# Performance work log

Hardware: AMD Instinct MI355X
Metric: run time of the kernel (lower is better)

The kernel has to match this reference:

```python
import jax, jax.numpy as jnp
import numpy as np

D_MODEL = 1024
N_HEADS = 16
NEG_INF = -1e9


def setup_inputs() -> dict:
    key = jax.random.key(0)
    ks = jax.random.split(key, 12)
    B, S, D = 2, 2048, D_MODEL
    Q = jax.random.normal(ks[0], (B, S, D), jnp.float32)
    K = jax.random.normal(ks[1], (B, S, D), jnp.float32)
    V = jax.random.normal(ks[2], (B, S, D), jnp.float32)
    # causal mask (1 = attend, 0 = masked), per mask==0 -> -1e9 in the source
    mask = jnp.tril(jnp.ones((S, S), bool))[None, :, :].repeat(B, axis=0)
    sc = 1.0 / np.sqrt(D)
    Wq = jax.random.normal(ks[3], (D, D), jnp.float32) * sc
    bq = jnp.zeros((D,), jnp.float32)
    Wk = jax.random.normal(ks[4], (D, D), jnp.float32) * sc
    bk = jnp.zeros((D,), jnp.float32)
    Wv = jax.random.normal(ks[5], (D, D), jnp.float32) * sc
    bv = jnp.zeros((D,), jnp.float32)
    Wo = jax.random.normal(ks[6], (D, D), jnp.float32) * sc
    bo = jnp.zeros((D,), jnp.float32)
    return {"Q": Q, "K": K, "V": V, "mask": mask,
            "Wq": Wq, "bq": bq, "Wk": Wk, "bk": bk,
            "Wv": Wv, "bv": bv, "Wo": Wo, "bo": bo}


def reference(Q, K, V, mask, Wq, bq, Wk, bk, Wv, bv, Wo, bo):
    B, S, D = Q.shape
    H = N_HEADS
    dk = D // H
    scale = jnp.asarray(dk, Q.dtype) ** -0.5
    # projections (torch nn.Linear: x @ W^T + b), split heads -> [B,H,S,dk]
    q = (Q @ Wq.T + bq).reshape(B, S, H, dk).transpose(0, 2, 1, 3)
    k = (K @ Wk.T + bk).reshape(B, S, H, dk).transpose(0, 2, 1, 3)
    v = (V @ Wv.T + bv).reshape(B, S, H, dk).transpose(0, 2, 1, 3)
    scores = jnp.einsum('bhqd,bhkd->bhqk', q, k) * scale  # [B,H,S,S]
    scores = jnp.where(mask[:, None, :, :], scores, NEG_INF)
    attn = jax.nn.softmax(scores, axis=-1)
    # dropout is identity in eval mode
    out = jnp.einsum('bhqk,bhkd->bhqd', attn, v)
    out = out.transpose(0, 2, 1, 3).reshape(B, S, D)
    return out @ Wo.T + bo, attn
```

## Files before the change

### kernel.cpp

```cpp
#include <hip/hip_runtime.h>
#include <cstddef>
#include <cstdint>

typedef unsigned short u16;
typedef unsigned int   u32;
typedef __attribute__((ext_vector_type(8))) short          bf16x8;
typedef __attribute__((ext_vector_type(4))) float          f32x4;
typedef __attribute__((ext_vector_type(4))) unsigned short u16x4;

#define S_LEN 2048
#define DM    1024
#define NROWS 4096
#define QSCALE 0.18033688011112042f
#define SOFTC  28.853900817779268f

__device__ __forceinline__ u16 f2bf(float x) {
  u32 u = __float_as_uint(x);
  return (u16)((u + 0x7fffu + ((u >> 16) & 1u)) >> 16);
}
__device__ __forceinline__ float bf2f(u16 h) { return __uint_as_float(((u32)h) << 16); }
__device__ __forceinline__ u32 cvtpk(float lo, float hi) {
  u32 r; asm("v_cvt_pk_bf16_f32 %0, %1, %2" : "=v"(r) : "v"(lo), "v"(hi)); return r;
}
__device__ __forceinline__ void gld16(const void* g, void* l) {
  __builtin_amdgcn_global_load_lds((const __attribute__((address_space(1))) void*)g,
                                   (__attribute__((address_space(3))) void*)l, 16, 0, 0);
}
__device__ __forceinline__ int swz4(int r) { return (r & 3) ^ ((r >> 2) & 3); }
#define MFMA16(a,b,c) __builtin_amdgcn_mfma_f32_16x16x32_bf16(a,b,c,0,0,0)

struct SplitArgs { const float* s[7]; u16* h[7]; u16* l[7]; int n4[7]; };

__global__ __launch_bounds__(256) void splitk7(SplitArgs a) {
  const int y = blockIdx.y;
  const float* s = a.s[y];
  u16* h = a.h[y]; u16* l = a.l[y];
  const int n4 = a.n4[y];
  const int step = gridDim.x * 256;
  for (int i = blockIdx.x * 256 + threadIdx.x; i < n4; i += step) {
    float4 v = ((const float4*)s)[i];
    u16x4 hh, ll; u16 x;
    x = f2bf(v.x); hh[0] = x; ll[0] = f2bf(v.x - bf2f(x));
    x = f2bf(v.y); hh[1] = x; ll[1] = f2bf(v.y - bf2f(x));
    x = f2bf(v.z); hh[2] = x; ll[2] = f2bf(v.z - bf2f(x));
    x = f2bf(v.w); hh[3] = x; ll[3] = f2bf(v.w - bf2f(x));
    *(u16x4*)&h[(size_t)i * 4] = hh;
    *(u16x4*)&l[(size_t)i * 4] = ll;
  }
}

template<int EPI>
__global__ __launch_bounds__(256) void gemm_split(
    const u16* __restrict__ Ah, const u16* __restrict__ Al,
    const u16* __restrict__ Bh, const u16* __restrict__ Bl,
    const float* __restrict__ bias,
    u16* __restrict__ Oh, u16* __restrict__ Ol, float* __restrict__ Of,
    float scale)
{
  __shared__ __align__(16) u16 lds[2][16384];
  const int t = threadIdx.x;
  const int id = blockIdx.x;
  const int bn = (id & 7) * 128;
  const int bm = (id >> 3) * 128;
  const int lane = t & 63, w = t >> 6;
  const int u = lane >> 4, c15 = lane & 15;
  const int wr = (w >> 1) * 64, wc = (w & 1) * 64;

  f32x4 acc[4][4];
#pragma unroll
  for (int i = 0; i < 4; ++i)
#pragma unroll
    for (int j = 0; j < 4; ++j) acc[i][j] = (f32x4){0.f, 0.f, 0.f, 0.f};

  auto stage = [&](int buf, int kb) {
    u16* L = lds[buf];
#pragma unroll
    for (int pp = 0; pp < 2; ++pp) {
      const int q = t + pp * 256;
      const int row = q >> 2;
      const int ch = (q & 3) ^ swz4(row);
      const int co = kb + 8 * ch;
      gld16(Ah + (size_t)(bm + row) * DM + co, L + q * 8);
      gld16(Al + (size_t)(bm + row) * DM + co, L + 4096 + q * 8);
      gld16(Bh + (size_t)(bn + row) * DM + co, L + 8192 + q * 8);
      gld16(Bl + (size_t)(bn + row) * DM + co, L + 12288 + q * 8);
    }
  };

  stage(0, 0);
  __syncthreads();
  int buf = 0;
  for (int kb = 0; kb < DM; kb += 32) {
    if (kb + 32 < DM) stage(buf ^ 1, kb + 32);
    const u16* L = lds[buf];
    bf16x8 ah[4], al[4];
#pragma unroll
    for (int i = 0; i < 4; ++i) {
      const int r = wr + 16 * i + c15;
      const int off = r * 32 + 8 * (u ^ swz4(r));
      ah[i] = *(const bf16x8*)&L[off];
      al[i] = *(const bf16x8*)&L[4096 + off];
    }
#pragma unroll
    for (int j = 0; j < 4; ++j) {
      const int n = wc + 16 * j + c15;
      const int off = n * 32 + 8 * (u ^ swz4(n));
      bf16x8 bh8 = *(const bf16x8*)&L[8192 + off];
      bf16x8 bl8 = *(const bf16x8*)&L[12288 + off];
#pragma unroll
      for (int i = 0; i < 4; ++i) {
        acc[i][j] = MFMA16(ah[i], bh8, acc[i][j]);
        acc[i][j] = MFMA16(ah[i], bl8, acc[i][j]);
        acc[i][j] = MFMA16(al[i], bh8, acc[i][j]);
      }
    }
    __syncthreads();
    buf ^= 1;
  }

#pragma unroll
  for (int j = 0; j < 4; ++j) {
    const int n = bn + wc + 16 * j + c15;
    const float bv = bias[n];
#pragma unroll
    for (int i = 0; i < 4; ++i) {
      float v[4];
#pragma unroll
      for (int r = 0; r < 4; ++r) v[r] = (acc[i][j][r] + bv) * scale;
      const int m0 = bm + wr + 16 * i + 4 * u;
      if (EPI == 2) {
#pragma unroll
        for (int r = 0; r < 4; ++r) Of[(size_t)(m0 + r) * DM + n] = v[r];
      } else if (EPI == 0) {
#pragma unroll
        for (int r = 0; r < 4; ++r) {
          const int m = m0 + r;
          const int b_ = m >> 11, s_ = m & 2047, h_ = n >> 6, d_ = n & 63;
          const size_t idx = (((size_t)(b_ * 16 + h_)) * S_LEN + s_) * 64 + d_;
          u16 hh = f2bf(v[r]);
          Oh[idx] = hh; Ol[idx] = f2bf(v[r] - bf2f(hh));
        }
      } else {
        u16x4 hv, lv;
#pragma unroll
        for (int r = 0; r < 4; ++r) {
          u16 hh = f2bf(v[r]); hv[r] = hh; lv[r] = f2bf(v[r] - bf2f(hh));
        }
        const int b_ = m0 >> 11, s_ = m0 & 2047, h_ = n >> 6, d_ = n & 63;
        const size_t idx = (((size_t)(b_ * 16 + h_)) * 64 + d_) * S_LEN + s_;
        *(u16x4*)&Oh[idx] = hv; *(u16x4*)&Ol[idx] = lv;
      }
    }
  }
}

__global__ __launch_bounds__(256) void attn_mfma(
    const u16* __restrict__ Qh, const u16* __restrict__ Ql,
    const u16* __restrict__ Kh, const u16* __restrict__ Kl,
    const u16* __restrict__ Vh, const u16* __restrict__ Vl,
    float* __restrict__ attnO, u16* __restrict__ Oh, u16* __restrict__ Ol)
{
  __shared__ __align__(16) u16 Kbuf[2][2][4096];
  __shared__ __align__(16) u16 Vbuf[2][4096];
  __shared__ __align__(16) float Pbuf[64][68];

  const int t = threadIdx.x;
  const int id = blockIdx.x;
  const int bh = (id & 7) * 4 + ((id >> 3) >> 4);
  const int pair = (id >> 3) & 15;
  const int lane = t & 63, w = t >> 6;
  const int u = lane >> 4, c15 = lane & 15;
  const size_t kvbase = (size_t)bh * S_LEN * 64;

  auto stageK = [&](int bb, int tk) {
    const int x = t >> 3, p = t & 7;
    const int co = 8 * (p ^ (x & 7));
    const u16* bH = Kh + kvbase + (size_t)tk * 4096;
    const u16* bL = Kl + kvbase + (size_t)tk * 4096;
    gld16(bH + (size_t)x * 64 + co,        &Kbuf[bb][0][t * 8]);
    gld16(bH + (size_t)(x + 32) * 64 + co, &Kbuf[bb][0][2048 + t * 8]);
    gld16(bL + (size_t)x * 64 + co,        &Kbuf[bb][1][t * 8]);
    gld16(bL + (size_t)(x + 32) * 64 + co, &Kbuf[bb][1][2048 + t * 8]);
  };
  auto stageV = [&](int tk) {
    const int x = t >> 3, p = t & 7;
    const int co = 8 * (p ^ (x & 7));
    const u16* bH = Vh + kvbase + (size_t)tk * 64;
    const u16* bL = Vl + kvbase + (size_t)tk * 64;
    gld16(bH + (size_t)x * S_LEN + co,        &Vbuf[0][t * 8]);
    gld16(bH + (size_t)(x + 32) * S_LEN + co, &Vbuf[0][2048 + t * 8]);
    gld16(bL + (size_t)x * S_LEN + co,        &Vbuf[1][t * 8]);
    gld16(bL + (size_t)(x + 32) * S_LEN + co, &Vbuf[1][2048 + t * 8]);
  };

  {
    const int rr0 = t >> 4, cq = t & 15;
    const float4 z = make_float4(0.f, 0.f, 0.f, 0.f);
#pragma unroll
    for (int which = 0; which < 2; ++which) {
      const int qb2 = which ? (31 - pair) : pair;
#pragma unroll
      for (int pp = 0; pp < 4; ++pp) {
        const int row = pp * 16 + rr0;
        float4* rowp = (float4*)(attnO + ((size_t)bh * S_LEN + qb2 * 64 + row) * S_LEN);
        for (int c4 = (qb2 + 1) * 16 + cq; c4 < 512; c4 += 16) rowp[c4] = z;
      }
    }
  }

  for (int which = 0; which < 2; ++which) {
    const int qb = which ? (31 - pair) : pair;
    const int q0 = qb * 64;

    const size_t qrow = kvbase + (size_t)(q0 + 16 * w + c15) * 64;
    bf16x8 qfh[2], qfl[2];
    qfh[0] = *(const bf16x8*)&Qh[qrow + 8 * u];
    qfh[1] = *(const bf16x8*)&Qh[qrow + 32 + 8 * u];
    qfl[0] = *(const bf16x8*)&Ql[qrow + 8 * u];
    qfl[1] = *(const bf16x8*)&Ql[qrow + 32 + 8 * u];

    float lsum[4] = {0.f, 0.f, 0.f, 0.f};

    int b = 0;
    stageK(0, 0);
    __syncthreads();
    for (int tk = 0; tk <= qb; ++tk) {
      if (tk < qb) stageK(b ^ 1, tk + 1);
      f32x4 sacc[4];
#pragma unroll
      for (int j = 0; j < 4; ++j) sacc[j] = (f32x4){0.f, 0.f, 0.f, 0.f};
      __builtin_amdgcn_s_setprio(1);
#pragma unroll
      for (int j = 0; j < 4; ++j) {
        const int srow = 16 * j + c15;
#pragma unroll
        for (int h = 0; h < 2; ++h) {
          const int off = srow * 64 + 8 * ((4 * h + u) ^ (srow & 7));
          bf16x8 kbh = *(const bf16x8*)&Kbuf[b][0][off];
          bf16x8 kbl = *(const bf16x8*)&Kbuf[b][1][off];
          sacc[j] = MFMA16(qfh[h], kbh, sacc[j]);
          sacc[j] = MFMA16(qfh[h], kbl, sacc[j]);
          sacc[j] = MFMA16(qfl[h], kbh, sacc[j]);
        }
      }
      __builtin_amdgcn_s_setprio(0);
      const bool dg = (tk == qb);
#pragma unroll
      for (int r = 0; r < 4; ++r) {
        const int qg = 16 * w + 4 * u + r;
#pragma unroll
        for (int j = 0; j < 4; ++j) {
          const int sg = tk * 64 + 16 * j + c15;
          const bool keep = (!dg) || (sg <= q0 + qg);
          lsum[r] += keep ? exp2f(sacc[j][r] - SOFTC) : 0.f;
        }
      }
      __syncthreads();
      b ^= 1;
    }

    float linv[4];
#pragma unroll
    for (int r = 0; r < 4; ++r) {
      float s = lsum[r];
      s += __shfl_xor(s, 1); s += __shfl_xor(s, 2);
      s += __shfl_xor(s, 4); s += __shfl_xor(s, 8);
      linv[r] = 1.0f / s;
    }

    b = 0;
    stageK(0, 0);
    __syncthreads();
    f32x4 oacc[4];
#pragma unroll
    for (int j = 0; j < 4; ++j) oacc[j] = (f32x4){0.f, 0.f, 0.f, 0.f};

    for (int tk = 0; tk <= qb; ++tk) {
      stageV(tk);
      if (tk < qb) stageK(b ^ 1, tk + 1);
      f32x4 sacc[4];
#pragma unroll
      for (int j = 0; j < 4; ++j) sacc[j] = (f32x4){0.f, 0.f, 0.f, 0.f};
      __builtin_amdgcn_s_setprio(1);
#pragma unroll
      for (int j = 0; j < 4; ++j) {
        const int srow = 16 * j + c15;
#pragma unroll
        for (int h = 0; h < 2; ++h) {
          const int off = srow * 64 + 8 * ((4 * h + u) ^ (srow & 7));
          bf16x8 kbh = *(const bf16x8*)&Kbuf[b][0][off];
          bf16x8 kbl = *(const bf16x8*)&Kbuf[b][1][off];
          sacc[j] = MFMA16(qfh[h], kbh, sacc[j]);
          sacc[j] = MFMA16(qfh[h], kbl, sacc[j]);
          sacc[j] = MFMA16(qfl[h], kbh, sacc[j]);
        }
      }
      __builtin_amdgcn_s_setprio(0);
      const bool dg = (tk == qb);
#pragma unroll
      for (int r = 0; r < 4; ++r) {
        const int qg = 16 * w + 4 * u + r;
        const float iv = linv[r];
#pragma unroll
        for (int j = 0; j < 4; ++j) {
          const int sl = 16 * j + c15;
          const int sg = tk * 64 + sl;
          const bool keep = (!dg) || (sg <= q0 + qg);
          Pbuf[qg][sl] = keep ? exp2f(sacc[j][r] - SOFTC) * iv : 0.f;
        }
      }
      __syncthreads();

      __builtin_amdgcn_s_setprio(1);
      {
        const int qloc = 16 * w + c15;
#pragma unroll
        for (int h = 0; h < 2; ++h) {
          f32x4 pa = *(const f32x4*)&Pbuf[qloc][32 * h + 8 * u];
          f32x4 pb = *(const f32x4*)&Pbuf[qloc][32 * h + 8 * u + 4];
          union { bf16x8 v; u32 x[4]; } H, L;
          H.x[0] = cvtpk(pa[0], pa[1]);
          H.x[1] = cvtpk(pa[2], pa[3]);
          H.x[2] = cvtpk(pb[0], pb[1]);
          H.x[3] = cvtpk(pb[2], pb[3]);
          float l0, l1;
          l0 = pa[0] - __uint_as_float(H.x[0] << 16);
          l1 = pa[1] - __uint_as_float(H.x[0] & 0xffff0000u);
          L.x[0] = cvtpk(l0, l1);
          l0 = pa[2] - __uint_as_float(H.x[1] << 16);
          l1 = pa[3] - __uint_as_float(H.x[1] & 0xffff0000u);
          L.x[1] = cvtpk(l0, l1);
          l0 = pb[0] - __uint_as_float(H.x[2] << 16);
          l1 = pb[1] - __uint_as_float(H.x[2] & 0xffff0000u);
          L.x[2] = cvtpk(l0, l1);
          l0 = pb[2] - __uint_as_float(H.x[3] << 16);
          l1 = pb[3] - __uint_as_float(H.x[3] & 0xffff0000u);
          L.x[3] = cvtpk(l0, l1);
#pragma unroll
          for (int j = 0; j < 4; ++j) {
            const int dr = 16 * j + c15;
            const int off = dr * 64 + 8 * ((4 * h + u) ^ (dr & 7));
            bf16x8 vH = *(const bf16x8*)&Vbuf[0][off];
            bf16x8 vL = *(const bf16x8*)&Vbuf[1][off];
            oacc[j] = MFMA16(H.v, vH, oacc[j]);
            oacc[j] = MFMA16(H.v, vL, oacc[j]);
            oacc[j] = MFMA16(L.v, vH, oacc[j]);
          }
        }
      }
      __builtin_amdgcn_s_setprio(0);

      {
        const int rr0 = t >> 4;
        const int cc = (t & 15) * 4;
        float* abase = attnO + ((size_t)bh * S_LEN + q0) * S_LEN + (size_t)tk * 64;
#pragma unroll
        for (int pp = 0; pp < 4; ++pp) {
          const int row = pp * 16 + rr0;
          f32x4 pv = *(const f32x4*)&Pbuf[row][cc];
          *(float4*)(abase + (size_t)row * S_LEN + cc) =
              make_float4(pv[0], pv[1], pv[2], pv[3]);
        }
      }
      __syncthreads();
      b ^= 1;
    }

    const int bb = bh >> 4, hh = bh & 15;
#pragma unroll
    for (int j = 0; j < 4; ++j) {
      const int d = 16 * j + c15;
#pragma unroll
      for (int r = 0; r < 4; ++r) {
        const int qg = q0 + 16 * w + 4 * u + r;
        const float v = oacc[j][r];
        const u16 hi = f2bf(v);
        const size_t idx = ((size_t)bb * S_LEN + qg) * DM + hh * 64 + d;
        Oh[idx] = hi; Ol[idx] = f2bf(v - bf2f(hi));
      }
    }
  }
}

extern "C" void kernel_launch(void* const* d_in, const int* in_sizes, int n_in,
                              void* d_out, int out_size, void* d_ws, size_t ws_size,
                              hipStream_t stream) {
  const float* Q  = (const float*)d_in[0];
  const float* K  = (const float*)d_in[1];
  const float* V  = (const float*)d_in[2];
  const float* Wq = (const float*)d_in[4];
  const float* bq = (const float*)d_in[5];
  const float* Wk = (const float*)d_in[6];
  const float* bk = (const float*)d_in[7];
  const float* Wv = (const float*)d_in[8];
  const float* bv = (const float*)d_in[9];
  const float* Wo = (const float*)d_in[10];
  const float* bo = (const float*)d_in[11];

  float* out  = (float*)d_out;
  float* attn = out + (size_t)NROWS * DM;

  u16* base = (u16*)d_ws;
  const size_t XN = (size_t)NROWS * DM;
  const size_t WN = (size_t)DM * DM;
  u16* xqh = base;       u16* xql = xqh + XN;
  u16* xkh = xql + XN;   u16* xkl = xkh + XN;
  u16* xvh = xkl + XN;   u16* xvl = xvh + XN;
  u16* wqh = xvl + XN;   u16* wql = wqh + WN;
  u16* wkh = wql + WN;   u16* wkl = wkh + WN;
  u16* wvh = wkl + WN;   u16* wvl = wvh + WN;
  u16* woh = wvl + WN;   u16* wol = woh + WN;
  u16* Qph = wol + WN;   u16* Qpl = Qph + XN;
  u16* Kph = Qpl + XN;   u16* Kpl = Kph + XN;
  u16* Vth = Kpl + XN;   u16* Vtl = Vth + XN;
  u16* Oh2 = Vtl + XN;   u16* Ol2 = Oh2 + XN;

  SplitArgs sa;
  sa.s[0] = Q;  sa.h[0] = xqh; sa.l[0] = xql; sa.n4[0] = (int)(XN / 4);
  sa.s[1] = K;  sa.h[1] = xkh; sa.l[1] = xkl; sa.n4[1] = (int)(XN / 4);
  sa.s[2] = V;  sa.h[2] = xvh; sa.l[2] = xvl; sa.n4[2] = (int)(XN / 4);
  sa.s[3] = Wq; sa.h[3] = wqh; sa.l[3] = wql; sa.n4[3] = (int)(WN / 4);
  sa.s[4] = Wk; sa.h[4] = wkh; sa.l[4] = wkl; sa.n4[4] = (int)(WN / 4);
  sa.s[5] = Wv; sa.h[5] = wvh; sa.l[5] = wvl; sa.n4[5] = (int)(WN / 4);
  sa.s[6] = Wo; sa.h[6] = woh; sa.l[6] = wol; sa.n4[6] = (int)(WN / 4);

  splitk7<<<dim3(1024, 7), 256, 0, stream>>>(sa);

  gemm_split<0><<<256, 256, 0, stream>>>(xqh, xql, wqh, wql, bq, Qph, Qpl, nullptr, QSCALE);
  gemm_split<0><<<256, 256, 0, stream>>>(xkh, xkl, wkh, wkl, bk, Kph, Kpl, nullptr, 1.0f);
  gemm_split<1><<<256, 256, 0, stream>>>(xvh, xvl, wvh, wvl, bv, Vth, Vtl, nullptr, 1.0f);

  attn_mfma<<<512, 256, 0, stream>>>(Qph, Qpl, Kph, Kpl, Vth, Vtl, attn, Oh2, Ol2);

  gemm_split<2><<<256, 256, 0, stream>>>(Oh2, Ol2, woh, wol, bo, nullptr, nullptr, out, 1.0f);
}
```

Measured before the change: 883.9 us.

## Switch split-bf16 compensated math to single fp16 MFMA and drop LDS staging

Replaces the hi/lo bf16 split (three MFMAs per product) with a single fp16 conversion and one fp16 MFMA per product in all GEMMs and attention. It removes the LDS staging and double buffering from the GEMM and attention kernels, loading operands straight from global memory. It also merges the three QKV projections into one launch and adds occupancy hints through launch bounds. This cuts MFMA work and memory traffic by about a factor of three, but loses precision (fp16 range and mantissa) and gives up the explicit LDS reuse, relying on caches instead.

New measurement: 934.7 us. +5.8%, slower.

```diff
diff --git a/kernel.cpp b/kernel.cpp
--- a/kernel.cpp
+++ b/kernel.cpp
@@ -4,9 +4,11 @@
 
 typedef unsigned short u16;
 typedef unsigned int   u32;
-typedef __attribute__((ext_vector_type(8))) short          bf16x8;
-typedef __attribute__((ext_vector_type(4))) float          f32x4;
-typedef __attribute__((ext_vector_type(4))) unsigned short u16x4;
+typedef _Float16 f16;
+typedef __attribute__((ext_vector_type(8))) _Float16 f16x8;
+typedef __attribute__((ext_vector_type(4))) _Float16 f16x4;
+typedef __attribute__((ext_vector_type(2))) __fp16   h16x2;
+typedef __attribute__((ext_vector_type(4))) float    f32x4;
 
 #define S_LEN 2048
 #define DM    1024
@@ -14,50 +16,32 @@
 #define QSCALE 0.18033688011112042f
 #define SOFTC  28.853900817779268f
 
-__device__ __forceinline__ u16 f2bf(float x) {
-  u32 u = __float_as_uint(x);
-  return (u16)((u + 0x7fffu + ((u >> 16) & 1u)) >> 16);
-}
-__device__ __forceinline__ float bf2f(u16 h) { return __uint_as_float(((u32)h) << 16); }
-__device__ __forceinline__ u32 cvtpk(float lo, float hi) {
-  u32 r; asm("v_cvt_pk_bf16_f32 %0, %1, %2" : "=v"(r) : "v"(lo), "v"(hi)); return r;
-}
-__device__ __forceinline__ void gld16(const void* g, void* l) {
-  __builtin_amdgcn_global_load_lds((const __attribute__((address_space(1))) void*)g,
-                                   (__attribute__((address_space(3))) void*)l, 16, 0, 0);
-}
-__device__ __forceinline__ int swz4(int r) { return (r & 3) ^ ((r >> 2) & 3); }
-#define MFMA16(a,b,c) __builtin_amdgcn_mfma_f32_16x16x32_bf16(a,b,c,0,0,0)
-
-struct SplitArgs { const float* s[7]; u16* h[7]; u16* l[7]; int n4[7]; };
-
-__global__ __launch_bounds__(256) void splitk7(SplitArgs a) {
+#define MFMA(a,b,c) __builtin_amdgcn_mfma_f32_16x16x32_f16(a,b,c,0,0,0)
+
+struct CvtArgs { const float* s[7]; f16* d[7]; int n8[7]; };
+
+__global__ __launch_bounds__(256) void cvt7(CvtArgs a) {
   const int y = blockIdx.y;
   const float* s = a.s[y];
-  u16* h = a.h[y]; u16* l = a.l[y];
-  const int n4 = a.n4[y];
+  f16* d = a.d[y];
+  const int n8 = a.n8[y];
   const int step = gridDim.x * 256;
-  for (int i = blockIdx.x * 256 + threadIdx.x; i < n4; i += step) {
-    float4 v = ((const float4*)s)[i];
-    u16x4 hh, ll; u16 x;
-    x = f2bf(v.x); hh[0] = x; ll[0] = f2bf(v.x - bf2f(x));
-    x = f2bf(v.y); hh[1] = x; ll[1] = f2bf(v.y - bf2f(x));
-    x = f2bf(v.z); hh[2] = x; ll[2] = f2bf(v.z - bf2f(x));
-    x = f2bf(v.w); hh[3] = x; ll[3] = f2bf(v.w - bf2f(x));
-    *(u16x4*)&h[(size_t)i * 4] = hh;
-    *(u16x4*)&l[(size_t)i * 4] = ll;
-  }
-}
-
-template<int EPI>
-__global__ __launch_bounds__(256) void gemm_split(
-    const u16* __restrict__ Ah, const u16* __restrict__ Al,
-    const u16* __restrict__ Bh, const u16* __restrict__ Bl,
+  for (int i = blockIdx.x * 256 + threadIdx.x; i < n8; i += step) {
+    float4 v0 = ((const float4*)s)[2 * i];
+    float4 v1 = ((const float4*)s)[2 * i + 1];
+    f16x8 o;
+    o[0] = (f16)v0.x; o[1] = (f16)v0.y; o[2] = (f16)v0.z; o[3] = (f16)v0.w;
+    o[4] = (f16)v1.x; o[5] = (f16)v1.y; o[6] = (f16)v1.z; o[7] = (f16)v1.w;
+    *(f16x8*)&d[(size_t)i * 8] = o;
+  }
+}
+
+__device__ __forceinline__ void gemm_body(
+    const f16* __restrict__ A, const f16* __restrict__ B,
     const float* __restrict__ bias,
-    u16* __restrict__ Oh, u16* __restrict__ Ol, float* __restrict__ Of,
-    float scale)
+    f16* __restrict__ Oh, float* __restrict__ Of,
+    float scale, int epi)
 {
-  __shared__ __align__(16) u16 lds[2][16384];
   const int t = threadIdx.x;
   const int id = blockIdx.x;
   const int bn = (id & 7) * 128;
@@ -72,50 +56,26 @@
 #pragma unroll
     for (int j = 0; j < 4; ++j) acc[i][j] = (f32x4){0.f, 0.f, 0.f, 0.f};
 
-  auto stage = [&](int buf, int kb) {
-    u16* L = lds[buf];
-#pragma unroll
-    for (int pp = 0; pp < 2; ++pp) {
-      const int q = t + pp * 256;
-      const int row = q >> 2;
-      const int ch = (q & 3) ^ swz4(row);
-      const int co = kb + 8 * ch;
-      gld16(Ah + (size_t)(bm + row) * DM + co, L + q * 8);
-      gld16(Al + (size_t)(bm + row) * DM + co, L + 4096 + q * 8);
-      gld16(Bh + (size_t)(bn + row) * DM + co, L + 8192 + q * 8);
-      gld16(Bl + (size_t)(bn + row) * DM + co, L + 12288 + q * 8);
-    }
-  };
-
-  stage(0, 0);
-  __syncthreads();
-  int buf = 0;
+  size_t abase[4], bbase[4];
+#pragma unroll
+  for (int i = 0; i < 4; ++i) {
+    abase[i] = (size_t)(bm + wr + 16 * i + c15) * DM;
+    bbase[i] = (size_t)(bn + wc + 16 * i + c15) * DM;
+  }
+
   for (int kb = 0; kb < DM; kb += 32) {
-    if (kb + 32 < DM) stage(buf ^ 1, kb + 32);
-    const u16* L = lds[buf];
-    bf16x8 ah[4], al[4];
+    const size_t k0 = (size_t)(kb + 8 * u);
+    f16x8 av[4], bv[4];
 #pragma unroll
     for (int i = 0; i < 4; ++i) {
-      const int r = wr + 16 * i + c15;
-      const int off = r * 32 + 8 * (u ^ swz4(r));
-      ah[i] = *(const bf16x8*)&L[off];
-      al[i] = *(const bf16x8*)&L[4096 + off];
-    }
-#pragma unroll
-    for (int j = 0; j < 4; ++j) {
-      const int n = wc + 16 * j + c15;
-      const int off = n * 32 + 8 * (u ^ swz4(n));
-      bf16x8 bh8 = *(const bf16x8*)&L[8192 + off];
-      bf16x8 bl8 = *(const bf16x8*)&L[12288 + off];
-#pragma unroll
-      for (int i = 0; i < 4; ++i) {
-        acc[i][j] = MFMA16(ah[i], bh8, acc[i][j]);
-        acc[i][j] = MFMA16(ah[i], bl8, acc[i][j]);
-        acc[i][j] = MFMA16(al[i], bh8, acc[i][j]);
-      }
-    }
-    __syncthreads();
-    buf ^= 1;
+      av[i] = *(const f16x8*)&A[abase[i] + k0];
+      bv[i] = *(const f16x8*)&B[bbase[i] + k0];
+    }
+#pragma unroll
+    for (int j = 0; j < 4; ++j)
+#pragma unroll
+      for (int i = 0; i < 4; ++i)
+        acc[i][j] = MFMA(av[i], bv[j], acc[i][j]);
   }
 
 #pragma unroll
@@ -128,40 +88,47 @@
 #pragma unroll
       for (int r = 0; r < 4; ++r) v[r] = (acc[i][j][r] + bv) * scale;
       const int m0 = bm + wr + 16 * i + 4 * u;
-      if (EPI == 2) {
+      if (epi == 2) {
 #pragma unroll
         for (int r = 0; r < 4; ++r) Of[(size_t)(m0 + r) * DM + n] = v[r];
-      } else if (EPI == 0) {
+      } else if (epi == 0) {
 #pragma unroll
         for (int r = 0; r < 4; ++r) {
           const int m = m0 + r;
           const int b_ = m >> 11, s_ = m & 2047, h_ = n >> 6, d_ = n & 63;
-          const size_t idx = (((size_t)(b_ * 16 + h_)) * S_LEN + s_) * 64 + d_;
-          u16 hh = f2bf(v[r]);
-          Oh[idx] = hh; Ol[idx] = f2bf(v[r] - bf2f(hh));
+          Oh[(((size_t)(b_ * 16 + h_)) * S_LEN + s_) * 64 + d_] = (f16)v[r];
         }
       } else {
-        u16x4 hv, lv;
-#pragma unroll
-        for (int r = 0; r < 4; ++r) {
-          u16 hh = f2bf(v[r]); hv[r] = hh; lv[r] = f2bf(v[r] - bf2f(hh));
-        }
+        f16x4 hv;
+#pragma unroll
+        for (int r = 0; r < 4; ++r) hv[r] = (f16)v[r];
         const int b_ = m0 >> 11, s_ = m0 & 2047, h_ = n >> 6, d_ = n & 63;
-        const size_t idx = (((size_t)(b_ * 16 + h_)) * 64 + d_) * S_LEN + s_;
-        *(u16x4*)&Oh[idx] = hv; *(u16x4*)&Ol[idx] = lv;
-      }
-    }
-  }
-}
-
-__global__ __launch_bounds__(256) void attn_mfma(
-    const u16* __restrict__ Qh, const u16* __restrict__ Ql,
-    const u16* __restrict__ Kh, const u16* __restrict__ Kl,
-    const u16* __restrict__ Vh, const u16* __restrict__ Vl,
-    float* __restrict__ attnO, u16* __restrict__ Oh, u16* __restrict__ Ol)
+        *(f16x4*)&Oh[(((size_t)(b_ * 16 + h_)) * 64 + d_) * S_LEN + s_] = hv;
+      }
+    }
+  }
+}
+
+struct QkvArgs {
+  const f16* A[3]; const f16* B[3]; const float* bias[3];
+  f16* O[3]; float scale[3]; int epi[3];
+};
+
+__global__ __launch_bounds__(256, 3) void gemm_qkv(QkvArgs a) {
+  const int y = blockIdx.y;
+  gemm_body(a.A[y], a.B[y], a.bias[y], a.O[y], nullptr, a.scale[y], a.epi[y]);
+}
+
+__global__ __launch_bounds__(256, 3) void gemm_out(
+    const f16* A, const f16* B, const float* bias, float* Of) {
+  gemm_body(A, B, bias, nullptr, Of, 1.0f, 2);
+}
+
+__global__ __launch_bounds__(256, 4) void attn_mfma(
+    const f16* __restrict__ Qh, const f16* __restrict__ Kh,
+    const f16* __restrict__ Vh,
+    float* __restrict__ attnO, f16* __restrict__ Op)
 {
-  __shared__ __align__(16) u16 Kbuf[2][2][4096];
-  __shared__ __align__(16) u16 Vbuf[2][4096];
   __shared__ __align__(16) float Pbuf[64][68];
 
   const int t = threadIdx.x;
@@ -170,28 +137,7 @@
   const int pair = (id >> 3) & 15;
   const int lane = t & 63, w = t >> 6;
   const int u = lane >> 4, c15 = lane & 15;
-  const size_t kvbase = (size_t)bh * S_LEN * 64;
-
-  auto stageK = [&](int bb, int tk) {
-    const int x = t >> 3, p = t & 7;
-    const int co = 8 * (p ^ (x & 7));
-    const u16* bH = Kh + kvbase + (size_t)tk * 4096;
-    const u16* bL = Kl + kvbase + (size_t)tk * 4096;
-    gld16(bH + (size_t)x * 64 + co,        &Kbuf[bb][0][t * 8]);
-    gld16(bH + (size_t)(x + 32) * 64 + co, &Kbuf[bb][0][2048 + t * 8]);
-    gld16(bL + (size_t)x * 64 + co,        &Kbuf[bb][1][t * 8]);
-    gld16(bL + (size_t)(x + 32) * 64 + co, &Kbuf[bb][1][2048 + t * 8]);
-  };
-  auto stageV = [&](int tk) {
-    const int x = t >> 3, p = t & 7;
-    const int co = 8 * (p ^ (x & 7));
-    const u16* bH = Vh + kvbase + (size_t)tk * 64;
-    const u16* bL = Vl + kvbase + (size_t)tk * 64;
-    gld16(bH + (size_t)x * S_LEN + co,        &Vbuf[0][t * 8]);
-    gld16(bH + (size_t)(x + 32) * S_LEN + co, &Vbuf[0][2048 + t * 8]);
-    gld16(bL + (size_t)x * S_LEN + co,        &Vbuf[1][t * 8]);
-    gld16(bL + (size_t)(x + 32) * S_LEN + co, &Vbuf[1][2048 + t * 8]);
-  };
+  const size_t kvbase = (size_t)bh * 131072;
 
   {
     const int rr0 = t >> 4, cq = t & 15;
@@ -213,34 +159,24 @@
     const int q0 = qb * 64;
 
     const size_t qrow = kvbase + (size_t)(q0 + 16 * w + c15) * 64;
-    bf16x8 qfh[2], qfl[2];
-    qfh[0] = *(const bf16x8*)&Qh[qrow + 8 * u];
-    qfh[1] = *(const bf16x8*)&Qh[qrow + 32 + 8 * u];
-    qfl[0] = *(const bf16x8*)&Ql[qrow + 8 * u];
-    qfl[1] = *(const bf16x8*)&Ql[qrow + 32 + 8 * u];
+    f16x8 qf[2];
+    qf[0] = *(const f16x8*)&Qh[qrow + 8 * u];
+    qf[1] = *(const f16x8*)&Qh[qrow + 32 + 8 * u];
 
     float lsum[4] = {0.f, 0.f, 0.f, 0.f};
 
-    int b = 0;
-    stageK(0, 0);
-    __syncthreads();
     for (int tk = 0; tk <= qb; ++tk) {
-      if (tk < qb) stageK(b ^ 1, tk + 1);
       f32x4 sacc[4];
 #pragma unroll
       for (int j = 0; j < 4; ++j) sacc[j] = (f32x4){0.f, 0.f, 0.f, 0.f};
       __builtin_amdgcn_s_setprio(1);
 #pragma unroll
       for (int j = 0; j < 4; ++j) {
-        const int srow = 16 * j + c15;
+        const size_t srow = kvbase + (size_t)(tk * 64 + 16 * j + c15) * 64;
 #pragma unroll
         for (int h = 0; h < 2; ++h) {
-          const int off = srow * 64 + 8 * ((4 * h + u) ^ (srow & 7));
-          bf16x8 kbh = *(const bf16x8*)&Kbuf[b][0][off];
-          bf16x8 kbl = *(const bf16x8*)&Kbuf[b][1][off];
-          sacc[j] = MFMA16(qfh[h], kbh, sacc[j]);
-          sacc[j] = MFMA16(qfh[h], kbl, sacc[j]);
-          sacc[j] = MFMA16(qfl[h], kbh, sacc[j]);
+          f16x8 kb8 = *(const f16x8*)&Kh[srow + 32 * h + 8 * u];
+          sacc[j] = MFMA(qf[h], kb8, sacc[j]);
         }
       }
       __builtin_amdgcn_s_setprio(0);
@@ -255,8 +191,6 @@
           lsum[r] += keep ? exp2f(sacc[j][r] - SOFTC) : 0.f;
         }
       }
-      __syncthreads();
-      b ^= 1;
     }
 
     float linv[4];
@@ -268,31 +202,22 @@
       linv[r] = 1.0f / s;
     }
 
-    b = 0;
-    stageK(0, 0);
-    __syncthreads();
     f32x4 oacc[4];
 #pragma unroll
     for (int j = 0; j < 4; ++j) oacc[j] = (f32x4){0.f, 0.f, 0.f, 0.f};
 
     for (int tk = 0; tk <= qb; ++tk) {
-      stageV(tk);
-      if (tk < qb) stageK(b ^ 1, tk + 1);
       f32x4 sacc[4];
 #pragma unroll
       for (int j = 0; j < 4; ++j) sacc[j] = (f32x4){0.f, 0.f, 0.f, 0.f};
       __builtin_amdgcn_s_setprio(1);
 #pragma unroll
       for (int j = 0; j < 4; ++j) {
-        const int srow = 16 * j + c15;
+        const size_t srow = kvbase + (size_t)(tk * 64 + 16 * j + c15) * 64;
 #pragma unroll
         for (int h = 0; h < 2; ++h) {
-          const int off = srow * 64 + 8 * ((4 * h + u) ^ (srow & 7));
-          bf16x8 kbh = *(const bf16x8*)&Kbuf[b][0][off];
-          bf16x8 kbl = *(const bf16x8*)&Kbuf[b][1][off];
-          sacc[j] = MFMA16(qfh[h], kbh, sacc[j]);
-          sacc[j] = MFMA16(qfh[h], kbl, sacc[j]);
-          sacc[j] = MFMA16(qfl[h], kbh, sacc[j]);
+          f16x8 kb8 = *(const f16x8*)&Kh[srow + 32 * h + 8 * u];
+          sacc[j] = MFMA(qf[h], kb8, sacc[j]);
         }
       }
       __builtin_amdgcn_s_setprio(0);
@@ -311,45 +236,6 @@
       }
       __syncthreads();
 
-      __builtin_amdgcn_s_setprio(1);
-      {
-        const int qloc = 16 * w + c15;
-#pragma unroll
-        for (int h = 0; h < 2; ++h) {
-          f32x4 pa = *(const f32x4*)&Pbuf[qloc][32 * h + 8 * u];
-          f32x4 pb = *(const f32x4*)&Pbuf[qloc][32 * h + 8 * u + 4];
-          union { bf16x8 v; u32 x[4]; } H, L;
-          H.x[0] = cvtpk(pa[0], pa[1]);
-          H.x[1] = cvtpk(pa[2], pa[3]);
-          H.x[2] = cvtpk(pb[0], pb[1]);
-          H.x[3] = cvtpk(pb[2], pb[3]);
-          float l0, l1;
-          l0 = pa[0] - __uint_as_float(H.x[0] << 16);
-          l1 = pa[1] - __uint_as_float(H.x[0] & 0xffff0000u);
-          L.x[0] = cvtpk(l0, l1);
-          l0 = pa[2] - __uint_as_float(H.x[1] << 16);
-          l1 = pa[3] - __uint_as_float(H.x[1] & 0xffff0000u);
-          L.x[1] = cvtpk(l0, l1);
-          l0 = pb[0] - __uint_as_float(H.x[2] << 16);
-          l1 = pb[1] - __uint_as_float(H.x[2] & 0xffff0000u);
-          L.x[2] = cvtpk(l0, l1);
-          l0 = pb[2] - __uint_as_float(H.x[3] << 16);
-          l1 = pb[3] - __uint_as_float(H.x[3] & 0xffff0000u);
-          L.x[3] = cvtpk(l0, l1);
-#pragma unroll
-          for (int j = 0; j < 4; ++j) {
-            const int dr = 16 * j + c15;
-            const int off = dr * 64 + 8 * ((4 * h + u) ^ (dr & 7));
-            bf16x8 vH = *(const bf16x8*)&Vbuf[0][off];
-            bf16x8 vL = *(const bf16x8*)&Vbuf[1][off];
-            oacc[j] = MFMA16(H.v, vH, oacc[j]);
-            oacc[j] = MFMA16(H.v, vL, oacc[j]);
-            oacc[j] = MFMA16(L.v, vH, oacc[j]);
-          }
-        }
-      }
-      __builtin_amdgcn_s_setprio(0);
-
       {
         const int rr0 = t >> 4;
         const int cc = (t & 15) * 4;
@@ -362,8 +248,30 @@
               make_float4(pv[0], pv[1], pv[2], pv[3]);
         }
       }
+
+      __builtin_amdgcn_s_setprio(1);
+      {
+        const int qloc = 16 * w + c15;
+#pragma unroll
+        for (int h = 0; h < 2; ++h) {
+          f32x4 pa = *(const f32x4*)&Pbuf[qloc][32 * h + 8 * u];
+          f32x4 pb = *(const f32x4*)&Pbuf[qloc][32 * h + 8 * u + 4];
+          union { f16x8 v; h16x2 h2[4]; } P;
+          P.h2[0] = __builtin_amdgcn_cvt_pkrtz(pa[0], pa[1]);
+          P.h2[1] = __builtin_amdgcn_cvt_pkrtz(pa[2], pa[3]);
+          P.h2[2] = __builtin_amdgcn_cvt_pkrtz(pb[0], pb[1]);
+          P.h2[3] = __builtin_amdgcn_cvt_pkrtz(pb[2], pb[3]);
+#pragma unroll
+          for (int j = 0; j < 4; ++j) {
+            const size_t drow = kvbase + (size_t)(16 * j + c15) * S_LEN
+                              + (size_t)tk * 64 + 32 * h + 8 * u;
+            f16x8 vH = *(const f16x8*)&Vh[drow];
+            oacc[j] = MFMA(P.v, vH, oacc[j]);
+          }
+        }
+      }
+      __builtin_amdgcn_s_setprio(0);
       __syncthreads();
-      b ^= 1;
     }
 
     const int bb = bh >> 4, hh = bh & 15;
@@ -373,10 +281,7 @@
 #pragma unroll
       for (int r = 0; r < 4; ++r) {
         const int qg = q0 + 16 * w + 4 * u + r;
-        const float v = oacc[j][r];
-        const u16 hi = f2bf(v);
-        const size_t idx = ((size_t)bb * S_LEN + qg) * DM + hh * 64 + d;
-        Oh[idx] = hi; Ol[idx] = f2bf(v - bf2f(hi));
+        Op[((size_t)bb * S_LEN + qg) * DM + hh * 64 + d] = (f16)oacc[j][r];
       }
     }
   }
@@ -400,37 +305,33 @@
   float* out  = (float*)d_out;
   float* attn = out + (size_t)NROWS * DM;
 
-  u16* base = (u16*)d_ws;
+  f16* base = (f16*)d_ws;
   const size_t XN = (size_t)NROWS * DM;
   const size_t WN = (size_t)DM * DM;
-  u16* xqh = base;       u16* xql = xqh + XN;
-  u16* xkh = xql + XN;   u16* xkl = xkh + XN;
-  u16* xvh = xkl + XN;   u16* xvl = xvh + XN;
-  u16* wqh = xvl + XN;   u16* wql = wqh + WN;
-  u16* wkh = wql + WN;   u16* wkl = wkh + WN;
-  u16* wvh = wkl + WN;   u16* wvl = wvh + WN;
-  u16* woh = wvl + WN;   u16* wol = woh + WN;
-  u16* Qph = wol + WN;   u16* Qpl = Qph + XN;
-  u16* Kph = Qpl + XN;   u16* Kpl = Kph + XN;
-  u16* Vth = Kpl + XN;   u16* Vtl = Vth + XN;
-  u16* Oh2 = Vtl + XN;   u16* Ol2 = Oh2 + XN;
-
-  SplitArgs sa;
-  sa.s[0] = Q;  sa.h[0] = xqh; sa.l[0] = xql; sa.n4[0] = (int)(XN / 4);
-  sa.s[1] = K;  sa.h[1] = xkh; sa.l[1] = xkl; sa.n4[1] = (int)(XN / 4);
-  sa.s[2] = V;  sa.h[2] = xvh; sa.l[2] = xvl; sa.n4[2] = (int)(XN / 4);
-  sa.s[3] = Wq; sa.h[3] = wqh; sa.l[3] = wql; sa.n4[3] = (int)(WN / 4);
-  sa.s[4] = Wk; sa.h[4] = wkh; sa.l[4] = wkl; sa.n4[4] = (int)(WN / 4);
-  sa.s[5] = Wv; sa.h[5] = wvh; sa.l[5] = wvl; sa.n4[5] = (int)(WN / 4);
-  sa.s[6] = Wo; sa.h[6] = woh; sa.l[6] = wol; sa.n4[6] = (int)(WN / 4);
-
-  splitk7<<<dim3(1024, 7), 256, 0, stream>>>(sa);
-
-  gemm_split<0><<<256, 256, 0, stream>>>(xqh, xql, wqh, wql, bq, Qph, Qpl, nullptr, QSCALE);
-  gemm_split<0><<<256, 256, 0, stream>>>(xkh, xkl, wkh, wkl, bk, Kph, Kpl, nullptr, 1.0f);
-  gemm_split<1><<<256, 256, 0, stream>>>(xvh, xvl, wvh, wvl, bv, Vth, Vtl, nullptr, 1.0f);
-
-  attn_mfma<<<512, 256, 0, stream>>>(Qph, Qpl, Kph, Kpl, Vth, Vtl, attn, Oh2, Ol2);
-
-  gemm_split<2><<<256, 256, 0, stream>>>(Oh2, Ol2, woh, wol, bo, nullptr, nullptr, out, 1.0f);
-}
+  f16* xq  = base;       f16* xk  = xq  + XN;
+  f16* xv  = xk  + XN;
+  f16* wq  = xv  + XN;   f16* wk  = wq  + WN;
+  f16* wv  = wk  + WN;   f16* wo  = wv  + WN;
+  f16* Qp  = wo  + WN;   f16* Kp  = Qp  + XN;
+  f16* Vt  = Kp  + XN;   f16* Op  = Vt  + XN;
+
+  CvtArgs ca;
+  ca.s[0] = Q;  ca.d[0] = xq; ca.n8[0] = (int)(XN / 8);
+  ca.s[1] = K;  ca.d[1] = xk; ca.n8[1] = (int)(XN / 8);
+  ca.s[2] = V;  ca.d[2] = xv; ca.n8[2] = (int)(XN / 8);
+  ca.s[3] = Wq; ca.d[3] = wq; ca.n8[3] = (int)(WN / 8);
+  ca.s[4] = Wk; ca.d[4] = wk; ca.n8[4] = (int)(WN / 8);
+  ca.s[5] = Wv; ca.d[5] = wv; ca.n8[5] = (int)(WN / 8);
+  ca.s[6] = Wo; ca.d[6] = wo; ca.n8[6] = (int)(WN / 8);
+  cvt7<<<dim3(512, 7), 256, 0, stream>>>(ca);
+
+  QkvArgs ga;
+  ga.A[0] = xq; ga.B[0] = wq; ga.bias[0] = bq; ga.O[0] = Qp; ga.scale[0] = QSCALE; ga.epi[0] = 0;
+  ga.A[1] = xk; ga.B[1] = wk; ga.bias[1] = bk; ga.O[1] = Kp; ga.scale[1] = 1.0f;   ga.epi[1] = 0;
+  ga.A[2] = xv; ga.B[2] = wv; ga.bias[2] = bv; ga.O[2] = Vt; ga.scale[2] = 1.0f;   ga.epi[2] = 1;
+  gemm_qkv<<<dim3(256, 3), 256, 0, stream>>>(ga);
+
+  attn_mfma<<<512, 256, 0, stream>>>(Qp, Kp, Vt, attn, Op);
+
+  gemm_out<<<256, 256, 0, stream>>>(Op, wo, bo, out);
+}
```
